# Performance work log

Measured on AMD Instinct MI355X. Metric: run time of the kernel, lower is better.

## Reference

```python
import jax, jax.numpy as jnp
import numpy as np

N, E, B = 128000, 512000, 128

def _conv1d(x, w, b):
    # x: [B,C,L], w: [O,I,K] (torch layout) -> valid conv, stride 1
    y = jax.lax.conv_general_dilated(x, w, (1,), 'VALID',
                                     dimension_numbers=('NCH', 'OIH', 'NCH'))
    return y + b[None, :, None]

def setup_inputs():
    key = jax.random.key(0)
    ks = jax.random.split(key, 22)
    def u(k, shape, fan_in):
        bound = 1.0 / np.sqrt(fan_in)
        return jax.random.uniform(k, shape, jnp.float32, -bound, bound)
    x = jax.random.normal(ks[0], (N, 33), jnp.float32)
    edge_index = jax.random.randint(ks[1], (2, E), 0, N, dtype=jnp.int64)
    batch = (jnp.arange(N, dtype=jnp.int64) * B) // N  # sorted, every graph non-empty
    target = jax.random.normal(ks[2], (B, 26, 1000), jnp.float32)
    return {
        'x': x, 'edge_index': edge_index, 'batch': batch, 'target': target,
        'lin_w': u(ks[3], (256, 33), 33), 'lin_b': jnp.zeros((256,), jnp.float32),
        'conv1_w': u(ks[4], (64, 26, 3), 26 * 3), 'conv1_b': u(ks[5], (64,), 26 * 3),
        'conv2_w': u(ks[6], (256, 64, 3), 64 * 3), 'conv2_b': u(ks[7], (256,), 64 * 3),
        'conv3_w': u(ks[8], (1024, 256, 5), 256 * 5), 'conv3_b': u(ks[9], (1024,), 256 * 5),
        'fc_w': u(ks[10], (768, 1024), 1024), 'fc_b': u(ks[11], (768,), 1024),
        'm1_w': u(ks[12], (1024, 1024), 1024), 'm1_b': u(ks[13], (1024,), 1024),
        'm2_w': u(ks[14], (1024, 1024), 1024), 'm2_b': u(ks[15], (1024,), 1024),
        'm3_w': u(ks[16], (512, 1024), 1024), 'm3_b': u(ks[17], (512,), 1024),
        'm4_w': u(ks[18], (1, 512), 512), 'm4_b': u(ks[19], (1,), 512),
    }

def reference(x, edge_index, batch, target,
              lin_w, lin_b, conv1_w, conv1_b, conv2_w, conv2_b,
              conv3_w, conv3_b, fc_w, fc_b,
              m1_w, m1_b, m2_w, m2_b, m3_w, m3_b, m4_w, m4_b):
    # ---- drug branch: GCN-normalized message passing, sum-aggr, graph mean ----
    xw = x @ lin_w.T                                   # [N,256]
    row, col = edge_index[0], edge_index[1]            # source j, target i
    deg = jax.ops.segment_sum(jnp.ones((E,), x.dtype), col, num_segments=N)
    dis = jnp.where(deg > 0, deg ** -0.5, 0.0)
    norm = dis[row] * dis[col]                         # [E]
    agg = jax.ops.segment_sum(norm[:, None] * xw[row], col, num_segments=N)
    out = agg + lin_b                                  # [N,256]
    sums = jax.ops.segment_sum(out, batch, num_segments=B)
    cnt = jax.ops.segment_sum(jnp.ones((N,), x.dtype), batch, num_segments=B)
    drug = jnp.where(cnt[:, None] > 0, sums / cnt[:, None], 0.0)  # [B,256]
    # ---- target branch: CNN (dropout = identity in eval) ----
    h = jax.nn.relu(_conv1d(target, conv1_w, conv1_b))
    h = jax.nn.relu(_conv1d(h, conv2_w, conv2_b))
    h = jax.nn.relu(_conv1d(h, conv3_w, conv3_b))
    h = jnp.max(h, axis=2)                             # AdaptiveMaxPool1d(1) -> [B,1024]
    tgt = jax.nn.relu(h @ fc_w.T + fc_b)               # [B,768]
    # ---- head MLP ----
    z = jnp.concatenate([drug, tgt], axis=1)           # [B,1024]
    z = jax.nn.relu(z @ m1_w.T + m1_b)
    z = jax.nn.relu(z @ m2_w.T + m2_b)
    z = jax.nn.relu(z @ m3_w.T + m3_b)
    return z @ m4_w.T + m4_b                           # [B,1]
```

## Files before the change

kernel.cpp:

```cpp
#include <hip/hip_runtime.h>

typedef unsigned short u16;
typedef __attribute__((ext_vector_type(8))) short short8;
typedef __attribute__((ext_vector_type(4))) float f32x4;

#define NN 128000
#define EE 512000
#define GB 128

#define GLDS16(g, l)                                                     \
  __builtin_amdgcn_global_load_lds(                                      \
      (const __attribute__((address_space(1))) unsigned int*)(g),        \
      (__attribute__((address_space(3))) unsigned int*)(l), 16, 0, 0)

__device__ __forceinline__ float u2f(u16 u) {
  union { unsigned u32; float f; } v; v.u32 = ((unsigned)u) << 16; return v.f;
}
__device__ __forceinline__ u16 f2bf(float x) {
  union { float f; unsigned u; } v; v.f = x;
  unsigned r = v.u + 0x7FFF + ((v.u >> 16) & 1);
  return (u16)(r >> 16);
}

__global__ void k_transpose(const float* lin_w, const float* w1, const float* w2, const float* w3,
                            float* lin_wT, float* w1T, u16* w2t, u16* w3p) {
  int idx = blockIdx.x * 256 + threadIdx.x;
  if (idx < 8448) { int i = idx >> 8, o = idx & 255; lin_wT[idx] = lin_w[o * 33 + i]; return; }
  idx -= 8448;
  if (idx < 4992) { int o = idx & 63, ck = idx >> 6; w1T[idx] = w1[o * 78 + ck]; return; }
  idx -= 4992;
  if (idx < 49152) {
    int c = idx & 63, o = (idx >> 6) & 255, k = idx >> 14;
    w2t[idx] = f2bf(w2[o * 192 + c * 3 + k]);
    return;
  }
  idx -= 49152;
  if (idx < 1310720) {
    int stcbk = idx >> 15;
    int fi    = (idx >> 9) & 63;
    int r512  = idx & 511;
    int quad  = r512 >> 7, l16 = (r512 >> 3) & 15, i = r512 & 7;
    int stcb  = stcbk / 5, k = stcbk - stcb * 5;
    int o = fi * 16 + l16;
    int c = stcb * 32 + quad * 8 + i;
    w3p[idx] = f2bf(w3[o * 1280 + c * 5 + k]);
  }
}

__global__ void k_deg_start(const int* ei, const int* batch, int* deg, int* start, int* hist) {
  __shared__ int lh[GB];
  int tid = threadIdx.x, blk = blockIdx.x;
  if (tid < GB) lh[tid] = 0;
  __syncthreads();
  int e0 = blk * 1024;
#pragma unroll
  for (int t = 0; t < 4; t++) {
    int e = e0 + t * 256 + tid;
    int col = ei[EE + e];
    atomicAdd(&deg[col], 1);
    atomicAdd(&lh[batch[col]], 1);
  }
  int i = blk * 256 + tid;
  int b = batch[i];
  if (i == 0) start[0] = 0;
  else if (b != batch[i - 1]) start[b] = i;
  if (i == NN - 1) start[GB] = NN;
  __syncthreads();
  if (tid < GB && lh[tid]) atomicAdd(&hist[tid * 16], lh[tid]);
}

__global__ void k_prefix(const int* hist, int* off, int* cursor) {
  __shared__ int h[GB];
  int tid = threadIdx.x;
  h[tid] = hist[tid * 16];
  __syncthreads();
  int s = 0;
  for (int j = 0; j < tid; j++) s += h[j];
  off[tid] = s;
  cursor[tid * 16] = s;
  if (tid == GB - 1) off[GB] = s + h[GB - 1];
}

__global__ void k_xw(const float* x, const float* lin_wT, const int* deg, u16* xw, float* dis) {
  __shared__ float xs[32][34];
  int tid = threadIdx.x, n0 = blockIdx.x * 32;
  int q = tid >> 6, lane = tid & 63;
  for (int n = q; n < 32; n += 4)
    if (lane < 33) xs[n][lane] = x[(n0 + n) * 33 + lane];
  float w[33];
#pragma unroll
  for (int i = 0; i < 33; i++) w[i] = lin_wT[i * 256 + tid];
  __syncthreads();
  for (int n = 0; n < 32; n++) {
    float acc = 0.f;
#pragma unroll
    for (int i = 0; i < 33; i++) acc += w[i] * xs[n][i];
    xw[(size_t)(n0 + n) * 256 + tid] = f2bf(acc);
  }
  if (tid < 32) { int d = deg[n0 + tid]; dis[n0 + tid] = d > 0 ? rsqrtf((float)d) : 0.f; }
}

__global__ void k_scatter(const int* ei, const int* batch, const float* dis,
                          int* cursor, uint2* bucket) {
  __shared__ int lh[GB];
  __shared__ int lbase[GB];
  int tid = threadIdx.x, blk = blockIdx.x;
  if (tid < GB) lh[tid] = 0;
  __syncthreads();
  int e0 = blk * 1024;
  int row[4], g[4], rk[4]; float nrm[4];
#pragma unroll
  for (int t = 0; t < 4; t++) {
    int e = e0 + t * 256 + tid;
    int r = ei[e], c = ei[EE + e];
    row[t] = r;
    g[t] = batch[c];
    nrm[t] = dis[r] * dis[c];
    rk[t] = atomicAdd(&lh[g[t]], 1);
  }
  __syncthreads();
  if (tid < GB && lh[tid]) lbase[tid] = atomicAdd(&cursor[tid * 16], lh[tid]);
  __syncthreads();
#pragma unroll
  for (int t = 0; t < 4; t++) {
    uint2 v; v.x = (unsigned)row[t]; v.y = __float_as_uint(nrm[t]);
    bucket[lbase[g[t]] + rk[t]] = v;
  }
}

__global__ void k_gather(const uint2* bucket, const int* off, const u16* xw, float* gsum) {
  __shared__ float red[4][256];
  int tid = threadIdx.x;
  int s = blockIdx.x, g = blockIdx.y;
  int lo = off[g], hi = off[g + 1];
  int cnt = hi - lo;
  int per = (cnt + 15) >> 4;
  int b0 = lo + s * per, b1 = min(b0 + per, hi);
  int lane = tid & 63, wid = tid >> 6;
  f32x4 acc = {0.f, 0.f, 0.f, 0.f};
  const u16* xbase = xw + lane * 4;
#pragma unroll 8
  for (int e = b0 + wid; e < b1; e += 4) {
    uint2 be = bucket[e];
    float nrm = __uint_as_float(be.y);
    ushort4 v = *(const ushort4*)(xbase + (size_t)be.x * 256);
    acc.x = fmaf(nrm, u2f(v.x), acc.x);
    acc.y = fmaf(nrm, u2f(v.y), acc.y);
    acc.z = fmaf(nrm, u2f(v.z), acc.z);
    acc.w = fmaf(nrm, u2f(v.w), acc.w);
  }
  *(f32x4*)&red[wid][lane * 4] = acc;
  __syncthreads();
  float v = red[0][tid] + red[1][tid] + red[2][tid] + red[3][tid];
  if (v != 0.f) atomicAdd(&gsum[tid * 128 + g], v);
}

__global__ void k_conv1(const float* target, const float* w1T, const float* b1, u16* h1T) {
  __shared__ float ts[26][132];
  __shared__ float wls[78 * 64];
  int tid = threadIdx.x, lt = blockIdx.x, bl = blockIdx.y;
  int l0 = lt * 128;
  int q = tid >> 6, lane = tid & 63;
  for (int c = q; c < 26; c += 4)
    for (int i = lane; i < 130; i += 64)
      ts[c][i] = target[(bl * 26 + c) * 1000 + min(l0 + i, 999)];
  for (int i = tid; i < 4992; i += 256) wls[i] = w1T[i];
  __syncthreads();
  int o = tid & 63, wid = tid >> 6;
  float w[78];
#pragma unroll
  for (int i = 0; i < 78; i++) w[i] = wls[i * 64 + o];
  float bias = b1[o];
  for (int t = 0; t < 32; t++) {
    int li = wid * 32 + t;
    float acc = bias;
#pragma unroll
    for (int c = 0; c < 26; c++)
#pragma unroll
      for (int k = 0; k < 3; k++) acc += ts[c][li + k] * w[c * 3 + k];
    int lg = l0 + li;
    if (lg < 998) h1T[((size_t)bl * 1000 + lg) * 64 + o] = f2bf(fmaxf(acc, 0.f));
  }
}

__global__ void k_conv2(const u16* h1T, const u16* w2t, const float* b2, u16* h2T) {
  __shared__ __align__(16) u16 als[132 * 32];
  __shared__ __align__(16) u16 bls[3 * 128 * 32];
  int tid = threadIdx.x;
  int lt = blockIdx.x, ot = blockIdx.y, bl = blockIdx.z;
  int l0 = lt * 128, o0 = ot * 128;
  int lane = tid & 63, wid = tid >> 6;
  int wm = wid >> 1, wn = wid & 1;
  int quad = lane >> 4, l16 = lane & 15;
  const f32x4 zero = {0.f, 0.f, 0.f, 0.f};
  f32x4 acc[4][4];
#pragma unroll
  for (int i = 0; i < 4; i++)
#pragma unroll
    for (int j = 0; j < 4; j++) acc[i][j] = zero;
  for (int cb = 0; cb < 2; cb++) {
    int c0 = cb * 32;
#pragma unroll
    for (int rr = 0; rr < 2; rr++) {
      int cid = rr * 256 + wid * 64 + lane;
      int row = cid >> 2, ch = (cid & 3) ^ (row & 3);
      GLDS16(h1T + ((size_t)bl * 1000 + min(l0 + row, 997)) * 64 + c0 + ch * 8,
             als + (rr * 256 + wid * 64) * 8);
    }
    if (wid == 0 && lane < 8) {
      int cid = 512 + lane;
      int row = cid >> 2, ch = (cid & 3) ^ (row & 3);
      GLDS16(h1T + ((size_t)bl * 1000 + min(l0 + row, 997)) * 64 + c0 + ch * 8, als + 512 * 8);
    }
#pragma unroll
    for (int rr = 0; rr < 6; rr++) {
      int cid = rr * 256 + wid * 64 + lane;
      int rko = cid >> 2, k = rko >> 7, o = rko & 127;
      int ch = (cid & 3) ^ (rko & 3);
      GLDS16(w2t + ((size_t)(k * 256 + o0 + o)) * 64 + c0 + ch * 8,
             bls + (rr * 256 + wid * 64) * 8);
    }
    __syncthreads();
#pragma unroll
    for (int k = 0; k < 3; k++) {
      short8 af[4], bfr[4];
#pragma unroll
      for (int i = 0; i < 4; i++) {
        int row = k + wm * 64 + i * 16 + l16;
        af[i] = *(const short8*)(als + row * 32 + ((quad ^ (row & 3)) * 8));
      }
#pragma unroll
      for (int j = 0; j < 4; j++) {
        int rowB = wn * 64 + j * 16 + l16;
        bfr[j] = *(const short8*)(bls + (k * 128 + rowB) * 32 + ((quad ^ (rowB & 3)) * 8));
      }
#pragma unroll
      for (int i = 0; i < 4; i++)
#pragma unroll
        for (int j = 0; j < 4; j++)
          acc[i][j] = __builtin_amdgcn_mfma_f32_16x16x32_bf16(af[i], bfr[j], acc[i][j], 0, 0, 0);
    }
    __syncthreads();
  }
#pragma unroll
  for (int j = 0; j < 4; j++) {
    int col = o0 + wn * 64 + j * 16 + l16;
    float bias = b2[col];
#pragma unroll
    for (int i = 0; i < 4; i++)
#pragma unroll
      for (int r = 0; r < 4; r++) {
        int lg = l0 + wm * 64 + i * 16 + quad * 4 + r;
        if (lg < 996)
          h2T[((size_t)bl * 996 + lg) * 256 + col] = f2bf(fmaxf(acc[i][j][r] + bias, 0.f));
      }
  }
}

__global__ void __launch_bounds__(256, 2)
k_conv3(const u16* h2T, const u16* w3p, const float* b3, float* pooledT) {
  __shared__ __align__(16) u16 als[2][1088 * 8];
  __shared__ float mbuf[256];
  int bid = blockIdx.x;
  int xc = bid & 7, rr0 = bid >> 3;
  int ot = rr0 & 3, bl = xc * 16 + (rr0 >> 2);
  int o0 = ot * 256;
  int tid = threadIdx.x;
  int lane = tid & 63, wn = tid >> 6;
  int quad = lane >> 4, l16 = lane & 15;
  float omax[4];
#pragma unroll
  for (int j = 0; j < 4; j++) omax[j] = -3.0e38f;
  const f32x4 zero = {0.f, 0.f, 0.f, 0.f};
  const u16* wb = w3p + (size_t)(ot * 16 + wn * 4) * 512 + lane * 8;
  const size_t rowbase = (size_t)bl * 996;

  {
    u16* dst = als[0];
#pragma unroll
    for (int c = 0; c < 4; c++) {
      int cid = c * 256 + tid;
      int row = cid >> 3, pp = cid & 7;
      int cc = (pp - row) & 7;
      GLDS16(h2T + (rowbase + min(row, 995)) * 256 + cc * 8, dst + cid * 8);
    }
    if (tid < 64) {
      int cid = 1024 + tid;
      int row = cid >> 3, pp = cid & 7;
      int cc = (pp - row) & 7;
      GLDS16(h2T + (rowbase + min(row, 995)) * 256 + cc * 8, dst + cid * 8);
    }
  }
  asm volatile("s_waitcnt vmcnt(0)" ::: "memory");
  __builtin_amdgcn_s_barrier();

  for (int lt = 0; lt < 8; lt++) {
    f32x4 acc[8][4];
#pragma unroll
    for (int i = 0; i < 8; i++)
#pragma unroll
      for (int j = 0; j < 4; j++) acc[i][j] = zero;
#pragma unroll 1
    for (int qc = 0; qc < 4; qc++) {
      const u16* a = als[qc & 1];
      {
        const u16* p_ = wb + (size_t)(qc * 2) * 5 * 32768;
        short8 breg[4];
        breg[0] = *(const short8*)(p_);
        breg[1] = *(const short8*)(p_ + 512);
        breg[2] = *(const short8*)(p_ + 1024);
        breg[3] = *(const short8*)(p_ + 1536);
#pragma unroll
        for (int i = 0; i < 8; i++) {
          int row = i * 16 + l16;
          int pp = (quad + row) & 7;
          short8 af = *(const short8*)(a + row * 64 + pp * 8);
          acc[i][0] = __builtin_amdgcn_mfma_f32_16x16x32_bf16(af, breg[0], acc[i][0], 0, 0, 0);
          acc[i][1] = __builtin_amdgcn_mfma_f32_16x16x32_bf16(af, breg[1], acc[i][1], 0, 0, 0);
          acc[i][2] = __builtin_amdgcn_mfma_f32_16x16x32_bf16(af, breg[2], acc[i][2], 0, 0, 0);
          acc[i][3] = __builtin_amdgcn_mfma_f32_16x16x32_bf16(af, breg[3], acc[i][3], 0, 0, 0);
        }
      }
      if (lt * 4 + qc < 31) {
        int nqc = (qc + 1) & 3;
        int nlt = lt + (qc == 3 ? 1 : 0);
        int l0n = nlt * 128;
        u16* dst = als[(qc + 1) & 1];
#pragma unroll
        for (int c = 0; c < 4; c++) {
          int cid = c * 256 + tid;
          int row = cid >> 3, pp = cid & 7;
          int cc = (pp - row) & 7;
          GLDS16(h2T + (rowbase + min(l0n + row, 995)) * 256 + nqc * 64 + cc * 8,
                 dst + cid * 8);
        }
        if (tid < 64) {
          int cid = 1024 + tid;
          int row = cid >> 3, pp = cid & 7;
          int cc = (pp - row) & 7;
          GLDS16(h2T + (rowbase + min(l0n + row, 995)) * 256 + nqc * 64 + cc * 8,
                 dst + cid * 8);
        }
      }
#pragma unroll 1
      for (int cbq = 0; cbq < 2; cbq++) {
        int stcb = qc * 2 + cbq;
        int k0 = (cbq == 0) ? 1 : 0;
#pragma unroll
        for (int k = k0; k < 5; k++) {
          const u16* p_ = wb + (size_t)(stcb * 5 + k) * 32768;
          short8 breg[4];
          breg[0] = *(const short8*)(p_);
          breg[1] = *(const short8*)(p_ + 512);
          breg[2] = *(const short8*)(p_ + 1024);
          breg[3] = *(const short8*)(p_ + 1536);
#pragma unroll
          for (int i = 0; i < 8; i++) {
            int row = k + i * 16 + l16;
            int pp = (cbq * 4 + quad + row) & 7;
            short8 af = *(const short8*)(a + row * 64 + pp * 8);
            acc[i][0] = __builtin_amdgcn_mfma_f32_16x16x32_bf16(af, breg[0], acc[i][0], 0, 0, 0);
            acc[i][1] = __builtin_amdgcn_mfma_f32_16x16x32_bf16(af, breg[1], acc[i][1], 0, 0, 0);
            acc[i][2] = __builtin_amdgcn_mfma_f32_16x16x32_bf16(af, breg[2], acc[i][2], 0, 0, 0);
            acc[i][3] = __builtin_amdgcn_mfma_f32_16x16x32_bf16(af, breg[3], acc[i][3], 0, 0, 0);
          }
        }
      }
      asm volatile("s_waitcnt vmcnt(0)" ::: "memory");
      __builtin_amdgcn_s_barrier();
    }
    int l0 = lt * 128;
#pragma unroll
    for (int i = 0; i < 8; i++) {
#pragma unroll
      for (int r = 0; r < 4; r++) {
        int lg = l0 + i * 16 + quad * 4 + r;
        if (lg < 992) {
#pragma unroll
          for (int j = 0; j < 4; j++) omax[j] = fmaxf(omax[j], acc[i][j][r]);
        }
      }
    }
  }
#pragma unroll
  for (int j = 0; j < 4; j++) {
    omax[j] = fmaxf(omax[j], __shfl_xor(omax[j], 16, 64));
    omax[j] = fmaxf(omax[j], __shfl_xor(omax[j], 32, 64));
  }
  if (quad == 0) {
#pragma unroll
    for (int j = 0; j < 4; j++) mbuf[wn * 64 + j * 16 + l16] = omax[j];
  }
  __syncthreads();
  {
    float v = mbuf[tid] + b3[o0 + tid];
    pooledT[(size_t)(o0 + tid) * 128 + bl] = fmaxf(v, 0.f);
  }
}

__global__ void k_z0(const float* gsum, const int* start, const float* lin_b, const float* tgtT,
                     float* z0T) {
  int idx = blockIdx.x * 256 + threadIdx.x;
  int r = idx >> 7, bb = idx & 127;
  float v;
  if (r < 256) {
    float c = (float)(start[bb + 1] - start[bb]);
    v = gsum[idx] / c + lin_b[r];
  } else {
    v = tgtT[(r - 256) * 128 + bb];
  }
  z0T[idx] = v;
}

__global__ void k_fc4(const float* zT, const float* W, const float* bias, float* outT,
                      int K, int O) {
  __shared__ float wls[4 * 1024];
  int tid = threadIdx.x;
  int o0 = blockIdx.x * 4;
  for (int idx = tid; idx < 4 * K; idx += 512) {
    int oo = idx / K, i = idx - oo * K;
    wls[oo * K + i] = W[(size_t)(o0 + oo) * K + i];
  }
  __syncthreads();
  int osub = tid >> 7, bb = tid & 127;
  int o = o0 + osub;
  float acc = 0.f;
  const float* wp = &wls[osub * K];
#pragma unroll 8
  for (int i = 0; i < K; i++) acc = fmaf(wp[i], zT[i * 128 + bb], acc);
  acc += bias[o];
  outT[(size_t)o * 128 + bb] = fmaxf(acc, 0.f);
}

__global__ void k_fc_final(const float* zT, const float* W, const float* bias, float* final_out,
                           int K) {
  __shared__ float wls[512];
  int tid = threadIdx.x;
  for (int i = tid; i < K; i += 256) wls[i] = W[i];
  __syncthreads();
  if (tid >= 128) return;
  int bb = tid;
  float acc = 0.f;
#pragma unroll 8
  for (int i = 0; i < K; i++) acc = fmaf(wls[i], zT[i * 128 + bb], acc);
  final_out[bb] = acc + bias[0];
}

extern "C" void kernel_launch(void* const* d_in, const int* in_sizes, int n_in,
                              void* d_out, int out_size, void* d_ws, size_t ws_size,
                              hipStream_t stream) {
  const float* x      = (const float*)d_in[0];
  const int*   ei     = (const int*)d_in[1];
  const int*   batch  = (const int*)d_in[2];
  const float* target = (const float*)d_in[3];
  const float* lin_w  = (const float*)d_in[4];
  const float* lin_b  = (const float*)d_in[5];
  const float* w1     = (const float*)d_in[6];
  const float* b1     = (const float*)d_in[7];
  const float* w2     = (const float*)d_in[8];
  const float* b2     = (const float*)d_in[9];
  const float* w3     = (const float*)d_in[10];
  const float* b3     = (const float*)d_in[11];
  const float* fcw    = (const float*)d_in[12];
  const float* fcb    = (const float*)d_in[13];
  const float* m1w = (const float*)d_in[14]; const float* m1b = (const float*)d_in[15];
  const float* m2w = (const float*)d_in[16]; const float* m2b = (const float*)d_in[17];
  const float* m3w = (const float*)d_in[18]; const float* m3b = (const float*)d_in[19];
  const float* m4w = (const float*)d_in[20]; const float* m4b = (const float*)d_in[21];

  char* ws = (char*)d_ws;
  size_t ofs = 0;
  auto alloc = [&](size_t bytes) -> void* {
    void* p = ws + ofs;
    ofs = (ofs + bytes + 255) & ~(size_t)255;
    return p;
  };
  int*   deg    = (int*)alloc((size_t)NN * 4);
  float* dis    = (float*)alloc((size_t)NN * 4);
  int*   start  = (int*)alloc((size_t)(GB + 1) * 4);
  int*   hist   = (int*)alloc((size_t)GB * 16 * 4);
  int*   off    = (int*)alloc((size_t)(GB + 1) * 4);
  int*   cursor = (int*)alloc((size_t)GB * 16 * 4);
  uint2* bucket = (uint2*)alloc((size_t)EE * 8);
  float* gsum   = (float*)alloc((size_t)256 * 128 * 4);
  float* lin_wT = (float*)alloc((size_t)33 * 256 * 4);
  float* w1T    = (float*)alloc((size_t)78 * 64 * 4);
  u16*   w2t    = (u16*)alloc((size_t)3 * 256 * 64 * 2);
  u16*   w3p    = (u16*)alloc((size_t)5 * 1024 * 256 * 2);
  float* pooledT= (float*)alloc((size_t)1024 * 128 * 4);
  float* tgtT   = (float*)alloc((size_t)768 * 128 * 4);
  float* z0T    = (float*)alloc((size_t)1024 * 128 * 4);
  float* z1T    = (float*)alloc((size_t)1024 * 128 * 4);
  float* z2T    = (float*)alloc((size_t)1024 * 128 * 4);
  float* z3T    = (float*)alloc((size_t)512 * 128 * 4);
  size_t F_end = ofs;

  u16* xw  = (u16*)(ws + F_end);
  u16* h1T = (u16*)(ws + F_end);
  u16* h2T = (u16*)(ws + F_end + (size_t)128 * 1000 * 64 * 2);

  hipMemsetAsync(deg, 0, (size_t)NN * 4, stream);
  hipMemsetAsync(hist, 0, (size_t)GB * 16 * 4, stream);
  hipMemsetAsync(gsum, 0, (size_t)256 * 128 * 4, stream);

  k_transpose<<<5365, 256, 0, stream>>>(lin_w, w1, w2, w3, lin_wT, w1T, w2t, w3p);
  k_deg_start<<<500, 256, 0, stream>>>(ei, batch, deg, start, hist);
  k_prefix<<<1, 128, 0, stream>>>(hist, off, cursor);
  k_xw<<<4000, 256, 0, stream>>>(x, lin_wT, deg, xw, dis);
  k_scatter<<<500, 256, 0, stream>>>(ei, batch, dis, cursor, bucket);
  k_gather<<<dim3(16, GB), 256, 0, stream>>>(bucket, off, xw, gsum);

  k_conv1<<<dim3(8, 128), 256, 0, stream>>>(target, w1T, b1, h1T);
  k_conv2<<<dim3(8, 2, 128), 256, 0, stream>>>(h1T, w2t, b2, h2T);
  k_conv3<<<512, 256, 0, stream>>>(h2T, w3p, b3, pooledT);

  k_fc4<<<192, 512, 0, stream>>>(pooledT, fcw, fcb, tgtT, 1024, 768);
  k_z0<<<512, 256, 0, stream>>>(gsum, start, lin_b, tgtT, z0T);
  k_fc4<<<256, 512, 0, stream>>>(z0T, m1w, m1b, z1T, 1024, 1024);
  k_fc4<<<256, 512, 0, stream>>>(z1T, m2w, m2b, z2T, 1024, 1024);
  k_fc4<<<128, 512, 0, stream>>>(z2T, m3w, m3b, z3T, 1024, 512);
  k_fc_final<<<1, 256, 0, stream>>>(z3T, m4w, m4b, (float*)d_out, 512);
}
```

Measured before the change: 827.1 us.

## Switch conv3 MFMA from 16x16x32 to 32x32x16 bf16 tiles

Rewrites the conv3 implicit-GEMM inner loop to use 32x32x16 bf16 MFMA instructions with a 4x2 tile of 32x32 accumulators per wave instead of 8x4 16x16 tiles. The weight prepack layout is changed to match the new B-operand lane mapping, and the max-pool reduction is adapted to the 32x32 output layout. The aim is fewer LDS A-fragment loads and fewer MFMA issues per FLOP, at the cost of a different register/accumulator layout. The tail masking changes from a per-row check to skipping the last whole 32-row tile, which relies on the 992-row boundary aligning with tile edges.

```diff
diff --git a/kernel.cpp b/kernel.cpp
--- a/kernel.cpp
+++ b/kernel.cpp
@@ -3,6 +3,7 @@
 typedef unsigned short u16;
 typedef __attribute__((ext_vector_type(8))) short short8;
 typedef __attribute__((ext_vector_type(4))) float f32x4;
+typedef __attribute__((ext_vector_type(16))) float f32x16;
 
 #define NN 128000
 #define EE 512000
@@ -36,14 +37,15 @@
   }
   idx -= 49152;
   if (idx < 1310720) {
-    int stcbk = idx >> 15;
-    int fi    = (idx >> 9) & 63;
-    int r512  = idx & 511;
-    int quad  = r512 >> 7, l16 = (r512 >> 3) & 15, i = r512 & 7;
-    int stcb  = stcbk / 5, k = stcbk - stcb * 5;
-    int o = fi * 16 + l16;
-    int c = stcb * 32 + quad * 8 + i;
-    w3p[idx] = f2bf(w3[o * 1280 + c * 5 + k]);
+    int sp   = idx >> 14;
+    int r    = idx & 16383;
+    int fi2  = r >> 9;
+    int r512 = r & 511;
+    int lh   = r512 >> 8, l31 = (r512 >> 3) & 31, i = r512 & 7;
+    int tap  = sp % 5, sk = sp / 5;
+    int o  = fi2 * 32 + l31;
+    int ch = sk * 16 + lh * 8 + i;
+    w3p[idx] = f2bf(w3[o * 1280 + ch * 5 + tap]);
   }
 }
 
@@ -267,12 +269,10 @@
   int o0 = ot * 256;
   int tid = threadIdx.x;
   int lane = tid & 63, wn = tid >> 6;
-  int quad = lane >> 4, l16 = lane & 15;
-  float omax[4];
-#pragma unroll
-  for (int j = 0; j < 4; j++) omax[j] = -3.0e38f;
-  const f32x4 zero = {0.f, 0.f, 0.f, 0.f};
-  const u16* wb = w3p + (size_t)(ot * 16 + wn * 4) * 512 + lane * 8;
+  int l31 = lane & 31, lh = lane >> 5;
+  float omax[2];
+  omax[0] = -3.0e38f; omax[1] = -3.0e38f;
+  const u16* wb = w3p + (size_t)(ot * 8 + wn * 2) * 512 + lane * 8;
   const size_t rowbase = (size_t)bl * 996;
 
   {
@@ -295,30 +295,27 @@
   __builtin_amdgcn_s_barrier();
 
   for (int lt = 0; lt < 8; lt++) {
-    f32x4 acc[8][4];
-#pragma unroll
-    for (int i = 0; i < 8; i++)
-#pragma unroll
-      for (int j = 0; j < 4; j++) acc[i][j] = zero;
+    f32x16 acc[4][2];
+#pragma unroll
+    for (int mt = 0; mt < 4; mt++)
+#pragma unroll
+      for (int nt = 0; nt < 2; nt++)
+#pragma unroll
+        for (int rg = 0; rg < 16; rg++) acc[mt][nt][rg] = 0.f;
 #pragma unroll 1
     for (int qc = 0; qc < 4; qc++) {
       const u16* a = als[qc & 1];
       {
-        const u16* p_ = wb + (size_t)(qc * 2) * 5 * 32768;
-        short8 breg[4];
-        breg[0] = *(const short8*)(p_);
-        breg[1] = *(const short8*)(p_ + 512);
-        breg[2] = *(const short8*)(p_ + 1024);
-        breg[3] = *(const short8*)(p_ + 1536);
-#pragma unroll
-        for (int i = 0; i < 8; i++) {
-          int row = i * 16 + l16;
-          int pp = (quad + row) & 7;
+        const u16* p_ = wb + (size_t)(qc * 20) * 16384;
+        short8 b0 = *(const short8*)(p_);
+        short8 b1 = *(const short8*)(p_ + 512);
+#pragma unroll
+        for (int mt = 0; mt < 4; mt++) {
+          int row = mt * 32 + l31;
+          int pp = (lh + row) & 7;
           short8 af = *(const short8*)(a + row * 64 + pp * 8);
-          acc[i][0] = __builtin_amdgcn_mfma_f32_16x16x32_bf16(af, breg[0], acc[i][0], 0, 0, 0);
-          acc[i][1] = __builtin_amdgcn_mfma_f32_16x16x32_bf16(af, breg[1], acc[i][1], 0, 0, 0);
-          acc[i][2] = __builtin_amdgcn_mfma_f32_16x16x32_bf16(af, breg[2], acc[i][2], 0, 0, 0);
-          acc[i][3] = __builtin_amdgcn_mfma_f32_16x16x32_bf16(af, breg[3], acc[i][3], 0, 0, 0);
+          acc[mt][0] = __builtin_amdgcn_mfma_f32_32x32x16_bf16(af, b0, acc[mt][0], 0, 0, 0);
+          acc[mt][1] = __builtin_amdgcn_mfma_f32_32x32x16_bf16(af, b1, acc[mt][1], 0, 0, 0);
         }
       }
       if (lt * 4 + qc < 31) {
@@ -343,53 +340,48 @@
         }
       }
 #pragma unroll 1
-      for (int cbq = 0; cbq < 2; cbq++) {
-        int stcb = qc * 2 + cbq;
-        int k0 = (cbq == 0) ? 1 : 0;
-#pragma unroll
-        for (int k = k0; k < 5; k++) {
-          const u16* p_ = wb + (size_t)(stcb * 5 + k) * 32768;
-          short8 breg[4];
-          breg[0] = *(const short8*)(p_);
-          breg[1] = *(const short8*)(p_ + 512);
-          breg[2] = *(const short8*)(p_ + 1024);
-          breg[3] = *(const short8*)(p_ + 1536);
-#pragma unroll
-          for (int i = 0; i < 8; i++) {
-            int row = k + i * 16 + l16;
-            int pp = (cbq * 4 + quad + row) & 7;
-            short8 af = *(const short8*)(a + row * 64 + pp * 8);
-            acc[i][0] = __builtin_amdgcn_mfma_f32_16x16x32_bf16(af, breg[0], acc[i][0], 0, 0, 0);
-            acc[i][1] = __builtin_amdgcn_mfma_f32_16x16x32_bf16(af, breg[1], acc[i][1], 0, 0, 0);
-            acc[i][2] = __builtin_amdgcn_mfma_f32_16x16x32_bf16(af, breg[2], acc[i][2], 0, 0, 0);
-            acc[i][3] = __builtin_amdgcn_mfma_f32_16x16x32_bf16(af, breg[3], acc[i][3], 0, 0, 0);
+      for (int cb = 0; cb < 2; cb++) {
+#pragma unroll
+        for (int tap = 0; tap < 5; tap++) {
+#pragma unroll
+          for (int ks = 0; ks < 2; ks++) {
+            if (cb == 0 && tap == 0 && ks == 0) continue;
+            int sp = (qc * 4 + cb * 2 + ks) * 5 + tap;
+            const u16* p_ = wb + (size_t)sp * 16384;
+            short8 b0 = *(const short8*)(p_);
+            short8 b1 = *(const short8*)(p_ + 512);
+            int ccb = cb * 4 + ks * 2 + lh;
+#pragma unroll
+            for (int mt = 0; mt < 4; mt++) {
+              int row = tap + mt * 32 + l31;
+              int pp = (ccb + row) & 7;
+              short8 af = *(const short8*)(a + row * 64 + pp * 8);
+              acc[mt][0] = __builtin_amdgcn_mfma_f32_32x32x16_bf16(af, b0, acc[mt][0], 0, 0, 0);
+              acc[mt][1] = __builtin_amdgcn_mfma_f32_32x32x16_bf16(af, b1, acc[mt][1], 0, 0, 0);
+            }
           }
         }
       }
       asm volatile("s_waitcnt vmcnt(0)" ::: "memory");
       __builtin_amdgcn_s_barrier();
     }
-    int l0 = lt * 128;
-#pragma unroll
-    for (int i = 0; i < 8; i++) {
-#pragma unroll
-      for (int r = 0; r < 4; r++) {
-        int lg = l0 + i * 16 + quad * 4 + r;
-        if (lg < 992) {
-#pragma unroll
-          for (int j = 0; j < 4; j++) omax[j] = fmaxf(omax[j], acc[i][j][r]);
+    int mtend = (lt == 7) ? 3 : 4;
+#pragma unroll
+    for (int mt = 0; mt < 4; mt++) {
+      if (mt < mtend) {
+#pragma unroll
+        for (int rg = 0; rg < 16; rg++) {
+          omax[0] = fmaxf(omax[0], acc[mt][0][rg]);
+          omax[1] = fmaxf(omax[1], acc[mt][1][rg]);
         }
       }
     }
   }
-#pragma unroll
-  for (int j = 0; j < 4; j++) {
-    omax[j] = fmaxf(omax[j], __shfl_xor(omax[j], 16, 64));
-    omax[j] = fmaxf(omax[j], __shfl_xor(omax[j], 32, 64));
-  }
-  if (quad == 0) {
-#pragma unroll
-    for (int j = 0; j < 4; j++) mbuf[wn * 64 + j * 16 + l16] = omax[j];
+  omax[0] = fmaxf(omax[0], __shfl_xor(omax[0], 32, 64));
+  omax[1] = fmaxf(omax[1], __shfl_xor(omax[1], 32, 64));
+  if (lane < 32) {
+    mbuf[wn * 64 + l31]      = omax[0];
+    mbuf[wn * 64 + 32 + l31] = omax[1];
   }
   __syncthreads();
   {
```

Result: slower. 1.445 ms (+74.7%).

## Reorder linear projection after graph aggregation to gather 33-wide features

Applied to the files above, without the earlier changes.

Since the GCN layer and the graph mean are both linear, the projection by lin_w is moved after aggregation. The kernel now gathers the raw 33-dim x rows into a per-graph [128,33] sum and applies lin_w in k_z0. This removes the k_xw kernel and its 128000x256 bf16 intermediate, and shrinks the gather traffic from 256 to 33 floats per edge. The degree normalisation is folded into k_scatter, removing the dis buffer, and gather threads beyond lane 33 sit idle.

```diff
diff --git a/kernel.cpp b/kernel.cpp
--- a/kernel.cpp
+++ b/kernel.cpp
@@ -22,11 +22,9 @@
   return (u16)(r >> 16);
 }
 
-__global__ void k_transpose(const float* lin_w, const float* w1, const float* w2, const float* w3,
-                            float* lin_wT, float* w1T, u16* w2t, u16* w3p) {
+__global__ void k_transpose(const float* w1, const float* w2, const float* w3,
+                            float* w1T, u16* w2t, u16* w3p) {
   int idx = blockIdx.x * 256 + threadIdx.x;
-  if (idx < 8448) { int i = idx >> 8, o = idx & 255; lin_wT[idx] = lin_w[o * 33 + i]; return; }
-  idx -= 8448;
   if (idx < 4992) { int o = idx & 63, ck = idx >> 6; w1T[idx] = w1[o * 78 + ck]; return; }
   idx -= 4992;
   if (idx < 49152) {
@@ -81,26 +79,7 @@
   if (tid == GB - 1) off[GB] = s + h[GB - 1];
 }
 
-__global__ void k_xw(const float* x, const float* lin_wT, const int* deg, u16* xw, float* dis) {
-  __shared__ float xs[32][34];
-  int tid = threadIdx.x, n0 = blockIdx.x * 32;
-  int q = tid >> 6, lane = tid & 63;
-  for (int n = q; n < 32; n += 4)
-    if (lane < 33) xs[n][lane] = x[(n0 + n) * 33 + lane];
-  float w[33];
-#pragma unroll
-  for (int i = 0; i < 33; i++) w[i] = lin_wT[i * 256 + tid];
-  __syncthreads();
-  for (int n = 0; n < 32; n++) {
-    float acc = 0.f;
-#pragma unroll
-    for (int i = 0; i < 33; i++) acc += w[i] * xs[n][i];
-    xw[(size_t)(n0 + n) * 256 + tid] = f2bf(acc);
-  }
-  if (tid < 32) { int d = deg[n0 + tid]; dis[n0 + tid] = d > 0 ? rsqrtf((float)d) : 0.f; }
-}
-
-__global__ void k_scatter(const int* ei, const int* batch, const float* dis,
+__global__ void k_scatter(const int* ei, const int* batch, const int* deg,
                           int* cursor, uint2* bucket) {
   __shared__ int lh[GB];
   __shared__ int lbase[GB];
@@ -115,7 +94,10 @@
     int r = ei[e], c = ei[EE + e];
     row[t] = r;
     g[t] = batch[c];
-    nrm[t] = dis[r] * dis[c];
+    int dr = deg[r], dc = deg[c];
+    float fr = dr > 0 ? rsqrtf((float)dr) : 0.f;
+    float fc = dc > 0 ? rsqrtf((float)dc) : 0.f;
+    nrm[t] = fr * fc;
     rk[t] = atomicAdd(&lh[g[t]], 1);
   }
   __syncthreads();
@@ -128,8 +110,8 @@
   }
 }
 
-__global__ void k_gather(const uint2* bucket, const int* off, const u16* xw, float* gsum) {
-  __shared__ float red[4][256];
+__global__ void k_gather33(const uint2* bucket, const int* off, const float* x, float* y) {
+  __shared__ float red[4][33];
   int tid = threadIdx.x;
   int s = blockIdx.x, g = blockIdx.y;
   int lo = off[g], hi = off[g + 1];
@@ -137,22 +119,21 @@
   int per = (cnt + 15) >> 4;
   int b0 = lo + s * per, b1 = min(b0 + per, hi);
   int lane = tid & 63, wid = tid >> 6;
-  f32x4 acc = {0.f, 0.f, 0.f, 0.f};
-  const u16* xbase = xw + lane * 4;
-#pragma unroll 8
-  for (int e = b0 + wid; e < b1; e += 4) {
-    uint2 be = bucket[e];
-    float nrm = __uint_as_float(be.y);
-    ushort4 v = *(const ushort4*)(xbase + (size_t)be.x * 256);
-    acc.x = fmaf(nrm, u2f(v.x), acc.x);
-    acc.y = fmaf(nrm, u2f(v.y), acc.y);
-    acc.z = fmaf(nrm, u2f(v.z), acc.z);
-    acc.w = fmaf(nrm, u2f(v.w), acc.w);
-  }
-  *(f32x4*)&red[wid][lane * 4] = acc;
-  __syncthreads();
-  float v = red[0][tid] + red[1][tid] + red[2][tid] + red[3][tid];
-  if (v != 0.f) atomicAdd(&gsum[tid * 128 + g], v);
+  float acc = 0.f;
+  if (lane < 33) {
+#pragma unroll 4
+    for (int e = b0 + wid; e < b1; e += 4) {
+      uint2 be = bucket[e];
+      float nrm = __uint_as_float(be.y);
+      acc = fmaf(nrm, x[(size_t)be.x * 33 + lane], acc);
+    }
+    red[wid][lane] = acc;
+  }
+  __syncthreads();
+  if (tid < 33) {
+    float v = red[0][tid] + red[1][tid] + red[2][tid] + red[3][tid];
+    if (v != 0.f) atomicAdd(&y[g * 33 + tid], v);
+  }
 }
 
 __global__ void k_conv1(const float* target, const float* w1T, const float* b1, u16* h1T) {
@@ -398,14 +379,19 @@
   }
 }
 
-__global__ void k_z0(const float* gsum, const int* start, const float* lin_b, const float* tgtT,
-                     float* z0T) {
+__global__ void k_z0(const float* y, const int* start, const float* lin_w, const float* lin_b,
+                     const float* tgtT, float* z0T) {
   int idx = blockIdx.x * 256 + threadIdx.x;
   int r = idx >> 7, bb = idx & 127;
   float v;
   if (r < 256) {
-    float c = (float)(start[bb + 1] - start[bb]);
-    v = gsum[idx] / c + lin_b[r];
+    float cnt = (float)(start[bb + 1] - start[bb]);
+    const float* yr = y + bb * 33;
+    const float* wr = lin_w + r * 33;
+    float acc = 0.f;
+#pragma unroll
+    for (int i = 0; i < 33; i++) acc = fmaf(yr[i], wr[i], acc);
+    v = acc / cnt + lin_b[r];
   } else {
     v = tgtT[(r - 256) * 128 + bb];
   }
@@ -476,14 +462,12 @@
     return p;
   };
   int*   deg    = (int*)alloc((size_t)NN * 4);
-  float* dis    = (float*)alloc((size_t)NN * 4);
   int*   start  = (int*)alloc((size_t)(GB + 1) * 4);
   int*   hist   = (int*)alloc((size_t)GB * 16 * 4);
   int*   off    = (int*)alloc((size_t)(GB + 1) * 4);
   int*   cursor = (int*)alloc((size_t)GB * 16 * 4);
   uint2* bucket = (uint2*)alloc((size_t)EE * 8);
-  float* gsum   = (float*)alloc((size_t)256 * 128 * 4);
-  float* lin_wT = (float*)alloc((size_t)33 * 256 * 4);
+  float* y      = (float*)alloc((size_t)GB * 33 * 4);
   float* w1T    = (float*)alloc((size_t)78 * 64 * 4);
   u16*   w2t    = (u16*)alloc((size_t)3 * 256 * 64 * 2);
   u16*   w3p    = (u16*)alloc((size_t)5 * 1024 * 256 * 2);
@@ -495,27 +479,25 @@
   float* z3T    = (float*)alloc((size_t)512 * 128 * 4);
   size_t F_end = ofs;
 
-  u16* xw  = (u16*)(ws + F_end);
   u16* h1T = (u16*)(ws + F_end);
   u16* h2T = (u16*)(ws + F_end + (size_t)128 * 1000 * 64 * 2);
 
   hipMemsetAsync(deg, 0, (size_t)NN * 4, stream);
   hipMemsetAsync(hist, 0, (size_t)GB * 16 * 4, stream);
-  hipMemsetAsync(gsum, 0, (size_t)256 * 128 * 4, stream);
-
-  k_transpose<<<5365, 256, 0, stream>>>(lin_w, w1, w2, w3, lin_wT, w1T, w2t, w3p);
+  hipMemsetAsync(y, 0, (size_t)GB * 33 * 4, stream);
+
+  k_transpose<<<5332, 256, 0, stream>>>(w1, w2, w3, w1T, w2t, w3p);
   k_deg_start<<<500, 256, 0, stream>>>(ei, batch, deg, start, hist);
   k_prefix<<<1, 128, 0, stream>>>(hist, off, cursor);
-  k_xw<<<4000, 256, 0, stream>>>(x, lin_wT, deg, xw, dis);
-  k_scatter<<<500, 256, 0, stream>>>(ei, batch, dis, cursor, bucket);
-  k_gather<<<dim3(16, GB), 256, 0, stream>>>(bucket, off, xw, gsum);
+  k_scatter<<<500, 256, 0, stream>>>(ei, batch, deg, cursor, bucket);
+  k_gather33<<<dim3(16, GB), 256, 0, stream>>>(bucket, off, x, y);
 
   k_conv1<<<dim3(8, 128), 256, 0, stream>>>(target, w1T, b1, h1T);
   k_conv2<<<dim3(8, 2, 128), 256, 0, stream>>>(h1T, w2t, b2, h2T);
   k_conv3<<<512, 256, 0, stream>>>(h2T, w3p, b3, pooledT);
 
   k_fc4<<<192, 512, 0, stream>>>(pooledT, fcw, fcb, tgtT, 1024, 768);
-  k_z0<<<512, 256, 0, stream>>>(gsum, start, lin_b, tgtT, z0T);
+  k_z0<<<512, 256, 0, stream>>>(y, start, lin_w, lin_b, tgtT, z0T);
   k_fc4<<<256, 512, 0, stream>>>(z0T, m1w, m1b, z1T, 1024, 1024);
   k_fc4<<<256, 512, 0, stream>>>(z1T, m2w, m2b, z2T, 1024, 1024);
   k_fc4<<<128, 512, 0, stream>>>(z2T, m3w, m3b, z3T, 1024, 512);
```

New measurement: 738.9 us. 10.7% less time.
